# Optimization experiments

Measured on AMD Instinct MI355X. Metric: run time of the kernel, lower is better.

The kernel has to match this reference:

```python
import jax, jax.numpy as jnp
import numpy as np
from jax import lax

B, T, I, H, O = 64, 512, 256, 1024, 1


def setup_inputs() -> dict:
    key = jax.random.key(0)
    ks = jax.random.split(key, 7)
    s_ih = 1.0 / np.sqrt(H)
    return {
        "x": jax.random.normal(ks[0], (B, T, I), dtype=jnp.float32),
        "W_ih": jax.random.uniform(ks[1], (4 * H, I), minval=-s_ih, maxval=s_ih, dtype=jnp.float32),
        "W_hh": jax.random.uniform(ks[2], (4 * H, H), minval=-s_ih, maxval=s_ih, dtype=jnp.float32),
        "b_ih": jax.random.uniform(ks[3], (4 * H,), minval=-s_ih, maxval=s_ih, dtype=jnp.float32),
        "b_hh": jax.random.uniform(ks[4], (4 * H,), minval=-s_ih, maxval=s_ih, dtype=jnp.float32),
        "fc_W": jax.random.uniform(ks[5], (O, H), minval=-s_ih, maxval=s_ih, dtype=jnp.float32),
        "fc_b": jax.random.uniform(ks[6], (O,), minval=-s_ih, maxval=s_ih, dtype=jnp.float32),
    }


def reference(x, W_ih, W_hh, b_ih, b_hh, fc_W, fc_b):
    Bd, Td, _ = x.shape
    Hd = W_hh.shape[1]
    # Precompute input projections for all timesteps: [T, B, 4H]
    x_proj = jnp.einsum('bti,gi->tbg', x, W_ih) + b_ih + b_hh

    def step(carry, xt):
        h, c = carry
        gates = xt + h @ W_hh.T  # [B, 4H]
        i_g, f_g, g_g, o_g = jnp.split(gates, 4, axis=-1)  # PyTorch order i,f,g,o
        i_g = jax.nn.sigmoid(i_g)
        f_g = jax.nn.sigmoid(f_g)
        g_g = jnp.tanh(g_g)
        o_g = jax.nn.sigmoid(o_g)
        c_new = f_g * c + i_g * g_g
        h_new = o_g * jnp.tanh(c_new)
        return (h_new, c_new), None

    h0 = jnp.zeros((Bd, Hd), dtype=x.dtype)
    c0 = jnp.zeros((Bd, Hd), dtype=x.dtype)
    (h_last, _), _ = lax.scan(step, (h0, c0), x_proj)
    out = jnp.tanh(h_last)          # tanh on last hidden state
    return out @ fc_W.T + fc_b      # [B, O]
```

## Files before the change

### kernel.cpp

```cpp
#include <hip/hip_runtime.h>
#include <hip/hip_bf16.h>


typedef __bf16 bf16_t;
typedef bf16_t b16x8 __attribute__((ext_vector_type(8)));
typedef float  f32x4 __attribute__((ext_vector_type(4)));

#define TQ 512
#define IQ 256
#define HQ 1024

union U8 { b16x8 b; unsigned long long q[2]; unsigned short u[8]; };

__device__ __forceinline__ float bf2f(unsigned short s) {
    return __uint_as_float(((unsigned)s) << 16);
}
__device__ __forceinline__ unsigned short f2bf(float f) {
    unsigned u = __float_as_uint(f);
    u += 0x7fff + ((u >> 16) & 1);
    return (unsigned short)(u >> 16);
}
__device__ __forceinline__ b16x8 cvt84(float4 a, float4 b) {
    U8 r;
    r.u[0] = f2bf(a.x); r.u[1] = f2bf(a.y); r.u[2] = f2bf(a.z); r.u[3] = f2bf(a.w);
    r.u[4] = f2bf(b.x); r.u[5] = f2bf(b.y); r.u[6] = f2bf(b.z); r.u[7] = f2bf(b.w);
    return r.b;
}
__device__ __forceinline__ b16x8 load_h16(const unsigned short* p) {
    U8 r;
    r.q[0] = __hip_atomic_load((const unsigned long long*)p,
                               __ATOMIC_RELAXED, __HIP_MEMORY_SCOPE_AGENT);
    r.q[1] = __hip_atomic_load((const unsigned long long*)(p + 4),
                               __ATOMIC_RELAXED, __HIP_MEMORY_SCOPE_AGENT);
    return r.b;
}
__device__ __forceinline__ float sigm(float x) {
    return 1.f / (1.f + __expf(-x));
}
__device__ __forceinline__ float tanh_f(float v) {
    float x = fminf(fmaxf(v, -15.f), 15.f);
    float e = __expf(2.f * x);
    return (e - 1.f) / (e + 1.f);
}

__launch_bounds__(512, 2)
__global__ void lstm_persist(const float* __restrict__ x,
                             const float* __restrict__ Wih,
                             const float* __restrict__ Whh,
                             const float* __restrict__ bih,
                             const float* __restrict__ bhh,
                             const float* __restrict__ fcW,
                             const float* __restrict__ fcb,
                             float* __restrict__ out,
                             unsigned short* __restrict__ hbuf,
                             unsigned int* __restrict__ bar)
{
    __shared__ float red[2 * 8192];

    const int tid  = threadIdx.x;
    const int w    = tid >> 6;
    const int lane = tid & 63;
    const int bid  = blockIdx.x;
    const int bg   = bid & 3;
    const int ug   = bid >> 2;

    const int l16  = lane & 15;
    const int quad = lane >> 4;

    b16x8 wih[4];
    b16x8 whh[4][4];
    {
        const int koff = quad * 8;
        #pragma unroll
        for (int g = 0; g < 4; ++g) {
            int row = g * HQ + ug * 16 + l16;
            const float* p = Wih + (size_t)row * IQ + w * 32 + koff;
            float4 a = *(const float4*)p;
            float4 b = *(const float4*)(p + 4);
            wih[g] = cvt84(a, b);
            #pragma unroll
            for (int j = 0; j < 4; ++j) {
                int k0 = (w * 4 + j) * 32 + koff;
                const float* q = Whh + (size_t)row * HQ + k0;
                float4 c = *(const float4*)q;
                float4 d = *(const float4*)(q + 4);
                whh[j][g] = cvt84(c, d);
            }
        }
    }

    float c_st[4] = {0.f, 0.f, 0.f, 0.f};
    float bias_r[4];
    if (w == 0) {
        #pragma unroll
        for (int g = 0; g < 4; ++g) {
            int gr = g * HQ + ug * 16 + l16;
            bias_r[g] = bih[gr] + bhh[gr];
        }
    }

    unsigned int* fl = bar + (size_t)bg * 1024;
    const unsigned int* myfl = fl + (size_t)(w * 8 + (lane & 7)) * 16;

    const float* xbase = x + ((size_t)(bg * 16 + l16) * TQ) * IQ + w * 32 + quad * 8;
    float4 xa = *(const float4*)(xbase);
    float4 xb = *(const float4*)(xbase + 4);

    for (int t = 0; t < TQ; ++t) {
        const int p = t & 1;

        b16x8 ax = cvt84(xa, xb);
        f32x4 acc[4];
        #pragma unroll
        for (int g = 0; g < 4; ++g) {
            f32x4 z = {0.f, 0.f, 0.f, 0.f};
            acc[g] = __builtin_amdgcn_mfma_f32_16x16x32_bf16(ax, wih[g], z, 0, 0, 0);
        }

        if (t) {
            unsigned tv = (unsigned)t;
            unsigned v = __hip_atomic_load(myfl, __ATOMIC_RELAXED,
                                           __HIP_MEMORY_SCOPE_AGENT);
            while (!__all(v >= tv))
                v = __hip_atomic_load(myfl, __ATOMIC_RELAXED,
                                      __HIP_MEMORY_SCOPE_AGENT);
        }

        const unsigned short* hread = hbuf + ((size_t)p * 4 + bg) * (16 * HQ);
        b16x8 ah[4];
        #pragma unroll
        for (int j = 0; j < 4; ++j)
            ah[j] = load_h16(hread + (size_t)l16 * HQ + (w * 4 + j) * 32 + quad * 8);
        #pragma unroll
        for (int j = 0; j < 4; ++j) {
            #pragma unroll
            for (int g = 0; g < 4; ++g)
                acc[g] = __builtin_amdgcn_mfma_f32_16x16x32_bf16(ah[j], whh[j][g], acc[g], 0, 0, 0);
        }

        float* rb = &red[p * 8192];
        #pragma unroll
        for (int g = 0; g < 4; ++g)
            *(f32x4*)&rb[((w * 4 + g) * 64 + lane) * 4] = acc[g];
        __syncthreads();

        if (w == 0) {
            f32x4 gv[4];
            #pragma unroll
            for (int g = 0; g < 4; ++g) {
                f32x4 s = *(const f32x4*)&rb[((0 * 4 + g) * 64 + lane) * 4];
                #pragma unroll
                for (int ww = 1; ww < 8; ++ww)
                    s += *(const f32x4*)&rb[((ww * 4 + g) * 64 + lane) * 4];
                gv[g] = s;
            }
            unsigned short* hw = hbuf + ((size_t)(p ^ 1) * 4 + bg) * (16 * HQ)
                               + (size_t)ug * 16 + l16;
            #pragma unroll
            for (int r = 0; r < 4; ++r) {
                float gi = gv[0][r] + bias_r[0];
                float gf = gv[1][r] + bias_r[1];
                float gg = gv[2][r] + bias_r[2];
                float go = gv[3][r] + bias_r[3];
                float i_s = sigm(gi);
                float f_s = sigm(gf);
                float g_t = tanh_f(gg);
                float o_s = sigm(go);
                float c = f_s * c_st[r] + i_s * g_t;
                c_st[r] = c;
                float h = o_s * tanh_f(c);
                int b = quad * 4 + r;
                __hip_atomic_store(hw + (size_t)b * HQ, f2bf(h),
                                   __ATOMIC_RELAXED, __HIP_MEMORY_SCOPE_AGENT);
            }
            asm volatile("s_waitcnt vmcnt(0)" ::: "memory");
            if (lane == 0)
                __hip_atomic_store(fl + (size_t)ug * 16, (unsigned)(t + 1),
                                   __ATOMIC_RELAXED, __HIP_MEMORY_SCOPE_AGENT);
            size_t nt = (t + 1 < TQ) ? (size_t)(t + 1) * IQ : (size_t)t * IQ;
            xa = *(const float4*)(xbase + nt);
            xb = *(const float4*)(xbase + nt + 4);
        } else {
            size_t nt = (t + 1 < TQ) ? (size_t)(t + 1) * IQ : (size_t)t * IQ;
            xa = *(const float4*)(xbase + nt);
            xb = *(const float4*)(xbase + nt + 4);
        }
    }

    if (bid < 4) {
        if (w == 0) {
            const unsigned int* pf = fl + (size_t)lane * 16;
            unsigned v = __hip_atomic_load(pf, __ATOMIC_RELAXED,
                                           __HIP_MEMORY_SCOPE_AGENT);
            while (!__all(v >= (unsigned)TQ))
                v = __hip_atomic_load(pf, __ATOMIC_RELAXED,
                                      __HIP_MEMORY_SCOPE_AGENT);
        }
        __syncthreads();
        const unsigned short* hl = hbuf + (size_t)bg * (16 * HQ);
        float fb = fcb[0];
        #pragma unroll
        for (int r = 0; r < 2; ++r) {
            int b = w * 2 + r;
            float s = 0.f;
            #pragma unroll
            for (int j = 0; j < 16; ++j) {
                int u = j * 64 + lane;
                unsigned short hv = __hip_atomic_load(hl + b * HQ + u,
                                                      __ATOMIC_RELAXED,
                                                      __HIP_MEMORY_SCOPE_AGENT);
                s += tanh_f(bf2f(hv)) * fcW[u];
            }
            #pragma unroll
            for (int off = 32; off > 0; off >>= 1)
                s += __shfl_down(s, off);
            if (lane == 0) out[bg * 16 + b] = s + fb;
        }
    }
}

extern "C" void kernel_launch(void* const* d_in, const int* in_sizes, int n_in,
                              void* d_out, int out_size, void* d_ws, size_t ws_size,
                              hipStream_t stream) {
    (void)in_sizes; (void)n_in; (void)out_size; (void)ws_size;
    const float* x   = (const float*)d_in[0];
    const float* Wih = (const float*)d_in[1];
    const float* Whh = (const float*)d_in[2];
    const float* bih = (const float*)d_in[3];
    const float* bhh = (const float*)d_in[4];
    const float* fcW = (const float*)d_in[5];
    const float* fcb = (const float*)d_in[6];
    float* out = (float*)d_out;

    unsigned short* hbuf = (unsigned short*)d_ws;
    unsigned int*   bar  = (unsigned int*)((char*)d_ws + 262144);

    hipMemsetAsync(d_ws, 0, 262144 + 16384, stream);

    void* args[] = { &x, &Wih, &Whh, &bih, &bhh, &fcW, &fcb, &out, &hbuf, &bar };
    hipLaunchCooperativeKernel(reinterpret_cast<void*>(lstm_persist),
                               dim3(256), dim3(512), args, 0, stream);
}
```

Before: 2.346 ms.

## Replace flag barrier with step-tagged hidden-state words for inter-block sync

Each hidden value is now stored as a 32-bit word holding the bf16 value in the low half and the timestep tag in the high half. Consumers poll the data words directly until every tag matches the current step, which removes the separate flag store, the vmcnt wait and the flag spin before loading h. The cost is double the hidden-state traffic and repolling of all 16 words on each retry. Sigmoid and tanh also switch from division to a hardware reciprocal.

```diff
diff --git a/kernel.cpp b/kernel.cpp
--- a/kernel.cpp
+++ b/kernel.cpp
@@ -10,7 +10,7 @@
 #define IQ 256
 #define HQ 1024
 
-union U8 { b16x8 b; unsigned long long q[2]; unsigned short u[8]; };
+union U8 { b16x8 b; unsigned long long q[2]; unsigned short u[8]; unsigned d[4]; };
 
 __device__ __forceinline__ float bf2f(unsigned short s) {
     return __uint_as_float(((unsigned)s) << 16);
@@ -26,21 +26,14 @@
     r.u[4] = f2bf(b.x); r.u[5] = f2bf(b.y); r.u[6] = f2bf(b.z); r.u[7] = f2bf(b.w);
     return r.b;
 }
-__device__ __forceinline__ b16x8 load_h16(const unsigned short* p) {
-    U8 r;
-    r.q[0] = __hip_atomic_load((const unsigned long long*)p,
-                               __ATOMIC_RELAXED, __HIP_MEMORY_SCOPE_AGENT);
-    r.q[1] = __hip_atomic_load((const unsigned long long*)(p + 4),
-                               __ATOMIC_RELAXED, __HIP_MEMORY_SCOPE_AGENT);
-    return r.b;
-}
+__device__ __forceinline__ float frcp(float x) { return __builtin_amdgcn_rcpf(x); }
 __device__ __forceinline__ float sigm(float x) {
-    return 1.f / (1.f + __expf(-x));
+    return frcp(1.f + __expf(-x));
 }
 __device__ __forceinline__ float tanh_f(float v) {
     float x = fminf(fmaxf(v, -15.f), 15.f);
     float e = __expf(2.f * x);
-    return (e - 1.f) / (e + 1.f);
+    return (e - 1.f) * frcp(e + 1.f);
 }
 
 __launch_bounds__(512, 2)
@@ -52,8 +45,7 @@
                              const float* __restrict__ fcW,
                              const float* __restrict__ fcb,
                              float* __restrict__ out,
-                             unsigned short* __restrict__ hbuf,
-                             unsigned int* __restrict__ bar)
+                             unsigned* __restrict__ hbuf)
 {
     __shared__ float red[2 * 8192];
 
@@ -83,8 +75,8 @@
                 int k0 = (w * 4 + j) * 32 + koff;
                 const float* q = Whh + (size_t)row * HQ + k0;
                 float4 c = *(const float4*)q;
-                float4 d = *(const float4*)(q + 4);
-                whh[j][g] = cvt84(c, d);
+                float4 e = *(const float4*)(q + 4);
+                whh[j][g] = cvt84(c, e);
             }
         }
     }
@@ -99,8 +91,8 @@
         }
     }
 
-    unsigned int* fl = bar + (size_t)bg * 1024;
-    const unsigned int* myfl = fl + (size_t)(w * 8 + (lane & 7)) * 16;
+    const unsigned* hrd0 = hbuf + ((size_t)bg * 16 + l16) * 1024 + w * 128 + quad * 8;
+    unsigned*       hwr0 = hbuf + (size_t)bg * 16384 + ug * 16 + l16;
 
     const float* xbase = x + ((size_t)(bg * 16 + l16) * TQ) * IQ + w * 32 + quad * 8;
     float4 xa = *(const float4*)(xbase);
@@ -108,6 +100,17 @@
 
     for (int t = 0; t < TQ; ++t) {
         const int p = t & 1;
+        const unsigned* hp = hrd0 + (size_t)p * 65536;
+
+        unsigned long long d[16];
+        #pragma unroll
+        for (int j = 0; j < 4; ++j) {
+            #pragma unroll
+            for (int k = 0; k < 4; ++k)
+                d[j * 4 + k] = __hip_atomic_load(
+                    (const unsigned long long*)(hp + j * 32 + k * 2),
+                    __ATOMIC_RELAXED, __HIP_MEMORY_SCOPE_AGENT);
+        }
 
         b16x8 ax = cvt84(xa, xb);
         f32x4 acc[4];
@@ -117,25 +120,36 @@
             acc[g] = __builtin_amdgcn_mfma_f32_16x16x32_bf16(ax, wih[g], z, 0, 0, 0);
         }
 
-        if (t) {
-            unsigned tv = (unsigned)t;
-            unsigned v = __hip_atomic_load(myfl, __ATOMIC_RELAXED,
-                                           __HIP_MEMORY_SCOPE_AGENT);
-            while (!__all(v >= tv))
-                v = __hip_atomic_load(myfl, __ATOMIC_RELAXED,
-                                      __HIP_MEMORY_SCOPE_AGENT);
-        }
-
-        const unsigned short* hread = hbuf + ((size_t)p * 4 + bg) * (16 * HQ);
-        b16x8 ah[4];
-        #pragma unroll
-        for (int j = 0; j < 4; ++j)
-            ah[j] = load_h16(hread + (size_t)l16 * HQ + (w * 4 + j) * 32 + quad * 8);
+        const unsigned need = (unsigned)t;
+        for (;;) {
+            unsigned m = 0xffffffffu;
+            #pragma unroll
+            for (int i = 0; i < 16; ++i) {
+                m &= (unsigned)d[i];
+                m &= (unsigned)(d[i] >> 32);
+            }
+            if (__all((m >> 16) == need)) break;
+            #pragma unroll
+            for (int j = 0; j < 4; ++j) {
+                #pragma unroll
+                for (int k = 0; k < 4; ++k)
+                    d[j * 4 + k] = __hip_atomic_load(
+                        (const unsigned long long*)(hp + j * 32 + k * 2),
+                        __ATOMIC_RELAXED, __HIP_MEMORY_SCOPE_AGENT);
+            }
+        }
+
         #pragma unroll
         for (int j = 0; j < 4; ++j) {
+            U8 r;
+            #pragma unroll
+            for (int mq = 0; mq < 4; ++mq)
+                r.d[mq] = __builtin_amdgcn_perm((unsigned)(d[j * 4 + mq] >> 32),
+                                                (unsigned)d[j * 4 + mq],
+                                                0x05040100u);
             #pragma unroll
             for (int g = 0; g < 4; ++g)
-                acc[g] = __builtin_amdgcn_mfma_f32_16x16x32_bf16(ah[j], whh[j][g], acc[g], 0, 0, 0);
+                acc[g] = __builtin_amdgcn_mfma_f32_16x16x32_bf16(r.b, whh[j][g], acc[g], 0, 0, 0);
         }
 
         float* rb = &red[p * 8192];
@@ -154,8 +168,8 @@
                     s += *(const f32x4*)&rb[((ww * 4 + g) * 64 + lane) * 4];
                 gv[g] = s;
             }
-            unsigned short* hw = hbuf + ((size_t)(p ^ 1) * 4 + bg) * (16 * HQ)
-                               + (size_t)ug * 16 + l16;
+            unsigned* hw = hwr0 + (size_t)(p ^ 1) * 65536;
+            const unsigned tagv = (unsigned)(t + 1) << 16;
             #pragma unroll
             for (int r = 0; r < 4; ++r) {
                 float gi = gv[0][r] + bias_r[0];
@@ -170,47 +184,37 @@
                 c_st[r] = c;
                 float h = o_s * tanh_f(c);
                 int b = quad * 4 + r;
-                __hip_atomic_store(hw + (size_t)b * HQ, f2bf(h),
+                __hip_atomic_store(hw + (size_t)b * 1024,
+                                   (unsigned)f2bf(h) | tagv,
                                    __ATOMIC_RELAXED, __HIP_MEMORY_SCOPE_AGENT);
             }
-            asm volatile("s_waitcnt vmcnt(0)" ::: "memory");
-            if (lane == 0)
-                __hip_atomic_store(fl + (size_t)ug * 16, (unsigned)(t + 1),
-                                   __ATOMIC_RELAXED, __HIP_MEMORY_SCOPE_AGENT);
-            size_t nt = (t + 1 < TQ) ? (size_t)(t + 1) * IQ : (size_t)t * IQ;
-            xa = *(const float4*)(xbase + nt);
-            xb = *(const float4*)(xbase + nt + 4);
-        } else {
-            size_t nt = (t + 1 < TQ) ? (size_t)(t + 1) * IQ : (size_t)t * IQ;
-            xa = *(const float4*)(xbase + nt);
-            xb = *(const float4*)(xbase + nt + 4);
-        }
+        }
+        size_t nt = (t + 1 < TQ) ? (size_t)(t + 1) * IQ : (size_t)t * IQ;
+        xa = *(const float4*)(xbase + nt);
+        xb = *(const float4*)(xbase + nt + 4);
     }
 
     if (bid < 4) {
-        if (w == 0) {
-            const unsigned int* pf = fl + (size_t)lane * 16;
-            unsigned v = __hip_atomic_load(pf, __ATOMIC_RELAXED,
-                                           __HIP_MEMORY_SCOPE_AGENT);
-            while (!__all(v >= (unsigned)TQ))
-                v = __hip_atomic_load(pf, __ATOMIC_RELAXED,
-                                      __HIP_MEMORY_SCOPE_AGENT);
-        }
-        __syncthreads();
-        const unsigned short* hl = hbuf + (size_t)bg * (16 * HQ);
+        const unsigned* hl = hbuf + (size_t)bg * 16384;
         float fb = fcb[0];
         #pragma unroll
         for (int r = 0; r < 2; ++r) {
             int b = w * 2 + r;
+            unsigned hv[16];
+            for (;;) {
+                #pragma unroll
+                for (int j = 0; j < 16; ++j)
+                    hv[j] = __hip_atomic_load(hl + (size_t)b * 1024 + j * 64 + lane,
+                                              __ATOMIC_RELAXED, __HIP_MEMORY_SCOPE_AGENT);
+                unsigned m = 0xffffffffu;
+                #pragma unroll
+                for (int j = 0; j < 16; ++j) m &= hv[j];
+                if (__all((m >> 16) == (unsigned)TQ)) break;
+            }
             float s = 0.f;
             #pragma unroll
-            for (int j = 0; j < 16; ++j) {
-                int u = j * 64 + lane;
-                unsigned short hv = __hip_atomic_load(hl + b * HQ + u,
-                                                      __ATOMIC_RELAXED,
-                                                      __HIP_MEMORY_SCOPE_AGENT);
-                s += tanh_f(bf2f(hv)) * fcW[u];
-            }
+            for (int j = 0; j < 16; ++j)
+                s += tanh_f(bf2f((unsigned short)hv[j])) * fcW[j * 64 + lane];
             #pragma unroll
             for (int off = 32; off > 0; off >>= 1)
                 s += __shfl_down(s, off);
@@ -232,12 +236,11 @@
     const float* fcb = (const float*)d_in[6];
     float* out = (float*)d_out;
 
-    unsigned short* hbuf = (unsigned short*)d_ws;
-    unsigned int*   bar  = (unsigned int*)((char*)d_ws + 262144);
-
-    hipMemsetAsync(d_ws, 0, 262144 + 16384, stream);
-
-    void* args[] = { &x, &Wih, &Whh, &bih, &bhh, &fcW, &fcb, &out, &hbuf, &bar };
+    unsigned* hbuf = (unsigned*)d_ws;
+
+    hipMemsetAsync(d_ws, 0, 524288, stream);
+
+    void* args[] = { &x, &Wih, &Whh, &bih, &bhh, &fcW, &fcb, &out, &hbuf };
     hipLaunchCooperativeKernel(reinterpret_cast<void*>(lstm_persist),
                                dim3(256), dim3(512), args, 0, stream);
 }
```

New measurement: 8.401 ms. 3.58x slower.

## Distribute gate reduction and cell update across all waves with per-wave flags

Applied to the files above, without the earlier changes.

The cross-wave reduction and LSTM cell update now run across all eight waves instead of only wave 0. Each wave reduces partial sums from a padded shared-memory layout for two batch rows and publishes its h values and its own ready flag. Consumers poll finer-grained per-wave flags, and divides in sigmoid and tanh are replaced by hardware reciprocal. The aim is to shorten the serial critical path of each timestep, at the cost of an extra __syncthreads per step and more flag polling.

```diff
diff --git a/kernel.cpp b/kernel.cpp
--- a/kernel.cpp
+++ b/kernel.cpp
@@ -9,6 +9,8 @@
 #define TQ 512
 #define IQ 256
 #define HQ 1024
+
+#define RED(w,g,u,b) (((((w)*4 + (g))*16 + (u))*20) + (b))
 
 union U8 { b16x8 b; unsigned long long q[2]; unsigned short u[8]; };
 
@@ -34,13 +36,14 @@
                                __ATOMIC_RELAXED, __HIP_MEMORY_SCOPE_AGENT);
     return r.b;
 }
+__device__ __forceinline__ float frcp(float x) { return __builtin_amdgcn_rcpf(x); }
 __device__ __forceinline__ float sigm(float x) {
-    return 1.f / (1.f + __expf(-x));
+    return frcp(1.f + __expf(-x));
 }
 __device__ __forceinline__ float tanh_f(float v) {
     float x = fminf(fmaxf(v, -15.f), 15.f);
     float e = __expf(2.f * x);
-    return (e - 1.f) / (e + 1.f);
+    return (e - 1.f) * frcp(e + 1.f);
 }
 
 __launch_bounds__(512, 2)
@@ -55,7 +58,7 @@
                              unsigned short* __restrict__ hbuf,
                              unsigned int* __restrict__ bar)
 {
-    __shared__ float red[2 * 8192];
+    __shared__ float red[8 * 4 * 16 * 20];
 
     const int tid  = threadIdx.x;
     const int w    = tid >> 6;
@@ -83,24 +86,28 @@
                 int k0 = (w * 4 + j) * 32 + koff;
                 const float* q = Whh + (size_t)row * HQ + k0;
                 float4 c = *(const float4*)q;
-                float4 d = *(const float4*)(q + 4);
-                whh[j][g] = cvt84(c, d);
+                float4 e = *(const float4*)(q + 4);
+                whh[j][g] = cvt84(c, e);
             }
         }
     }
 
-    float c_st[4] = {0.f, 0.f, 0.f, 0.f};
-    float bias_r[4];
-    if (w == 0) {
-        #pragma unroll
-        for (int g = 0; g < 4; ++g) {
-            int gr = g * HQ + ug * 16 + l16;
-            bias_r[g] = bih[gr] + bhh[gr];
-        }
-    }
-
-    unsigned int* fl = bar + (size_t)bg * 1024;
-    const unsigned int* myfl = fl + (size_t)(w * 8 + (lane & 7)) * 16;
+    const int hi  = (lane >> 5) & 1;
+    const int eb  = 2 * w + hi;
+    const int dup = (lane >> 4) & 1;
+    float c_st = 0.f;
+    float bias_g[4];
+    #pragma unroll
+    for (int g = 0; g < 4; ++g) {
+        int gr = g * HQ + ug * 16 + l16;
+        bias_g[g] = bih[gr] + bhh[gr];
+    }
+
+    const unsigned short* hrd0 = hbuf + ((size_t)bg * 16 + l16) * HQ;
+    unsigned short*       hwr0 = hbuf + (size_t)bg * 16 * HQ + (size_t)eb * HQ + ug * 16 + l16;
+
+    const unsigned int* myfl = bar + ((size_t)(bg * 64 + w * 8 + (lane >> 3)) * 16 + (lane & 7));
+    unsigned int*       wfl  = bar + ((size_t)(bg * 64 + ug) * 16 + w);
 
     const float* xbase = x + ((size_t)(bg * 16 + l16) * TQ) * IQ + w * 32 + quad * 8;
     float4 xa = *(const float4*)(xbase);
@@ -117,20 +124,20 @@
             acc[g] = __builtin_amdgcn_mfma_f32_16x16x32_bf16(ax, wih[g], z, 0, 0, 0);
         }
 
-        if (t) {
-            unsigned tv = (unsigned)t;
+        const unsigned need = (unsigned)t;
+        {
             unsigned v = __hip_atomic_load(myfl, __ATOMIC_RELAXED,
                                            __HIP_MEMORY_SCOPE_AGENT);
-            while (!__all(v >= tv))
+            while (!__all(v >= need))
                 v = __hip_atomic_load(myfl, __ATOMIC_RELAXED,
                                       __HIP_MEMORY_SCOPE_AGENT);
         }
 
-        const unsigned short* hread = hbuf + ((size_t)p * 4 + bg) * (16 * HQ);
+        const unsigned short* hread = hrd0 + (size_t)p * (4 * 16 * HQ);
         b16x8 ah[4];
         #pragma unroll
         for (int j = 0; j < 4; ++j)
-            ah[j] = load_h16(hread + (size_t)l16 * HQ + (w * 4 + j) * 32 + quad * 8);
+            ah[j] = load_h16(hread + (w * 4 + j) * 32 + quad * 8);
         #pragma unroll
         for (int j = 0; j < 4; ++j) {
             #pragma unroll
@@ -138,83 +145,78 @@
                 acc[g] = __builtin_amdgcn_mfma_f32_16x16x32_bf16(ah[j], whh[j][g], acc[g], 0, 0, 0);
         }
 
-        float* rb = &red[p * 8192];
+        __syncthreads();
+
         #pragma unroll
         for (int g = 0; g < 4; ++g)
-            *(f32x4*)&rb[((w * 4 + g) * 64 + lane) * 4] = acc[g];
+            *(f32x4*)&red[RED(w, g, l16, quad * 4)] = acc[g];
         __syncthreads();
 
-        if (w == 0) {
-            f32x4 gv[4];
-            #pragma unroll
-            for (int g = 0; g < 4; ++g) {
-                f32x4 s = *(const f32x4*)&rb[((0 * 4 + g) * 64 + lane) * 4];
-                #pragma unroll
-                for (int ww = 1; ww < 8; ++ww)
-                    s += *(const f32x4*)&rb[((ww * 4 + g) * 64 + lane) * 4];
-                gv[g] = s;
-            }
-            unsigned short* hw = hbuf + ((size_t)(p ^ 1) * 4 + bg) * (16 * HQ)
-                               + (size_t)ug * 16 + l16;
-            #pragma unroll
-            for (int r = 0; r < 4; ++r) {
-                float gi = gv[0][r] + bias_r[0];
-                float gf = gv[1][r] + bias_r[1];
-                float gg = gv[2][r] + bias_r[2];
-                float go = gv[3][r] + bias_r[3];
-                float i_s = sigm(gi);
-                float f_s = sigm(gf);
-                float g_t = tanh_f(gg);
-                float o_s = sigm(go);
-                float c = f_s * c_st[r] + i_s * g_t;
-                c_st[r] = c;
-                float h = o_s * tanh_f(c);
-                int b = quad * 4 + r;
-                __hip_atomic_store(hw + (size_t)b * HQ, f2bf(h),
+        float s[4];
+        #pragma unroll
+        for (int g = 0; g < 4; ++g) {
+            float a0 = red[RED(dup * 4 + 0, g, l16, eb)]
+                     + red[RED(dup * 4 + 1, g, l16, eb)];
+            float a1 = red[RED(dup * 4 + 2, g, l16, eb)]
+                     + red[RED(dup * 4 + 3, g, l16, eb)];
+            float as = a0 + a1;
+            as += __shfl_xor(as, 16);
+            s[g] = as;
+        }
+        {
+            float gi = s[0] + bias_g[0];
+            float gf = s[1] + bias_g[1];
+            float gg = s[2] + bias_g[2];
+            float go = s[3] + bias_g[3];
+            float i_s = sigm(gi);
+            float f_s = sigm(gf);
+            float g_t = tanh_f(gg);
+            float o_s = sigm(go);
+            float c = f_s * c_st + i_s * g_t;
+            c_st = c;
+            float h = o_s * tanh_f(c);
+            if (!dup)
+                __hip_atomic_store(hwr0 + (size_t)(p ^ 1) * (4 * 16 * HQ), f2bf(h),
                                    __ATOMIC_RELAXED, __HIP_MEMORY_SCOPE_AGENT);
-            }
-            asm volatile("s_waitcnt vmcnt(0)" ::: "memory");
-            if (lane == 0)
-                __hip_atomic_store(fl + (size_t)ug * 16, (unsigned)(t + 1),
-                                   __ATOMIC_RELAXED, __HIP_MEMORY_SCOPE_AGENT);
-            size_t nt = (t + 1 < TQ) ? (size_t)(t + 1) * IQ : (size_t)t * IQ;
-            xa = *(const float4*)(xbase + nt);
-            xb = *(const float4*)(xbase + nt + 4);
-        } else {
-            size_t nt = (t + 1 < TQ) ? (size_t)(t + 1) * IQ : (size_t)t * IQ;
-            xa = *(const float4*)(xbase + nt);
-            xb = *(const float4*)(xbase + nt + 4);
-        }
+        }
+        asm volatile("s_waitcnt vmcnt(0)" ::: "memory");
+        if (lane == 0)
+            __hip_atomic_store(wfl, (unsigned)(t + 1),
+                               __ATOMIC_RELAXED, __HIP_MEMORY_SCOPE_AGENT);
+
+        size_t nt = (t + 1 < TQ) ? (size_t)(t + 1) * IQ : (size_t)t * IQ;
+        xa = *(const float4*)(xbase + nt);
+        xb = *(const float4*)(xbase + nt + 4);
     }
 
     if (bid < 4) {
-        if (w == 0) {
-            const unsigned int* pf = fl + (size_t)lane * 16;
+        #pragma unroll
+        for (int pb = 0; pb < 8; ++pb) {
+            const unsigned int* pf = bar + ((size_t)(bg * 64 + pb * 8 + (lane >> 3)) * 16 + (lane & 7));
             unsigned v = __hip_atomic_load(pf, __ATOMIC_RELAXED,
                                            __HIP_MEMORY_SCOPE_AGENT);
             while (!__all(v >= (unsigned)TQ))
                 v = __hip_atomic_load(pf, __ATOMIC_RELAXED,
                                       __HIP_MEMORY_SCOPE_AGENT);
         }
-        __syncthreads();
-        const unsigned short* hl = hbuf + (size_t)bg * (16 * HQ);
+        const unsigned short* hl = hbuf + (size_t)bg * 16 * HQ;
         float fb = fcb[0];
         #pragma unroll
         for (int r = 0; r < 2; ++r) {
             int b = w * 2 + r;
-            float s = 0.f;
+            float sacc = 0.f;
             #pragma unroll
             for (int j = 0; j < 16; ++j) {
                 int u = j * 64 + lane;
-                unsigned short hv = __hip_atomic_load(hl + b * HQ + u,
+                unsigned short hv = __hip_atomic_load(hl + (size_t)b * HQ + u,
                                                       __ATOMIC_RELAXED,
                                                       __HIP_MEMORY_SCOPE_AGENT);
-                s += tanh_f(bf2f(hv)) * fcW[u];
+                sacc += tanh_f(bf2f(hv)) * fcW[u];
             }
             #pragma unroll
             for (int off = 32; off > 0; off >>= 1)
-                s += __shfl_down(s, off);
-            if (lane == 0) out[bg * 16 + b] = s + fb;
+                sacc += __shfl_down(sacc, off);
+            if (lane == 0) out[bg * 16 + b] = sacc + fb;
         }
     }
 }
```

After: 2.250 ms. 1.04x faster.
